# Kernel tuning notes

Measured on AMD Instinct MI355X. Metric: run time of the kernel, lower is better.

The kernel has to match this reference:

```python
import jax, jax.numpy as jnp
import numpy as np

LN_EPS = 1e-5
ALPHA_Q = 1.0

def _ln(t, g, b):
    mu = jnp.mean(t, -1, keepdims=True)
    var = jnp.var(t, -1, keepdims=True)
    return (t - mu) / jnp.sqrt(var + LN_EPS) * g + b

def _mlp(t, w1, b1, w2, b2):
    h = jax.nn.gelu(t @ w1.T + b1, approximate=False)
    return h @ w2.T + b2

def setup_inputs() -> dict:
    key = jax.random.key(0)
    B, N, L, E, H, D = 2, 2048, 2048, 1024, 16, 4
    ks = jax.random.split(key, 40)
    rn = lambda i, shape, sc: jax.random.normal(ks[i], shape, jnp.float32) * sc
    inp = {}
    inp['x'] = rn(0, (B, N, E), 1.0)
    inp['xp'] = jax.random.uniform(ks[1], (B, N, D), jnp.float32)
    inp['y'] = rn(2, (B, L, E), 1.0)
    inp['yp'] = jax.random.uniform(ks[3], (B, L, D), jnp.float32)
    inp['attn_mask'] = jax.random.uniform(ks[4], (1, 1, N, L), jnp.float32)
    # PositionEncoder params (torch Linear convention: weight [out,in])
    inp['p_w1'] = rn(5, (E, D), 1.0 / D)
    inp['p_b1'] = jax.random.uniform(ks[6], (E,), jnp.float32, 0.0, np.pi)
    inp['p_w2'] = rn(7, (E, D), 1.0 / D)
    inp['p_b2'] = jax.random.uniform(ks[8], (E,), jnp.float32, 0.0, np.pi)
    # QueryEncoder: LayerNorm + mlp1 + mlp2 (mlp0 is dead code in the source)
    inp['q_ln_g'] = jnp.ones((E,), jnp.float32); inp['q_ln_b'] = jnp.zeros((E,), jnp.float32)
    inp['q_m1_w1'] = rn(9, (2 * E, E), 0.02); inp['q_m1_b1'] = jnp.zeros((2 * E,), jnp.float32)
    inp['q_m1_w2'] = rn(10, (E, 2 * E), 0.02); inp['q_m1_b2'] = jnp.zeros((E,), jnp.float32)
    inp['q_m2_w1'] = rn(11, (2 * E, E), 0.02); inp['q_m2_b1'] = jnp.zeros((2 * E,), jnp.float32)
    inp['q_m2_w2'] = rn(12, (E, 2 * E), 0.02); inp['q_m2_b2'] = jnp.zeros((E,), jnp.float32)
    # KeyEncoder: LayerNorm + mlp1 (mlp0 dead code)
    inp['k_ln_g'] = jnp.ones((E,), jnp.float32); inp['k_ln_b'] = jnp.zeros((E,), jnp.float32)
    inp['k_m1_w1'] = rn(13, (2 * E, E), 0.02); inp['k_m1_b1'] = jnp.zeros((2 * E,), jnp.float32)
    inp['k_m1_w2'] = rn(14, (E, 2 * E), 0.02); inp['k_m1_b2'] = jnp.zeros((E,), jnp.float32)
    # V: LayerNorm + Linear
    inp['v_ln_g'] = jnp.ones((E,), jnp.float32); inp['v_ln_b'] = jnp.zeros((E,), jnp.float32)
    inp['v_w'] = rn(15, (E, E), 0.02); inp['v_b'] = jnp.zeros((E,), jnp.float32)
    # output projections
    inp['proj1_w'] = rn(16, (E, E), 0.02); inp['proj1_b'] = jnp.zeros((E,), jnp.float32)
    inp['proj2_w'] = rn(17, (E, D * H), 0.02); inp['proj2_b'] = jnp.zeros((E,), jnp.float32)
    return inp

def reference(x, xp, y, yp, attn_mask, p_w1, p_b1, p_w2, p_b2,
              q_ln_g, q_ln_b, q_m1_w1, q_m1_b1, q_m1_w2, q_m1_b2,
              q_m2_w1, q_m2_b1, q_m2_w2, q_m2_b2,
              k_ln_g, k_ln_b, k_m1_w1, k_m1_b1, k_m1_w2, k_m1_b2,
              v_ln_g, v_ln_b, v_w, v_b, proj1_w, proj1_b, proj2_w, proj2_b):
    B, N, E = x.shape
    L = y.shape[1]
    D = xp.shape[2]
    H = proj2_w.shape[1] // D
    C = E // H
    # PositionEncoder: query side with bias, key side without bias
    pxt = ALPHA_Q * xp
    xp1 = pxt @ p_w1.T + p_b1            # [B,N,E]
    xp2 = pxt @ p_w2.T + p_b2
    pyt = ALPHA_Q * yp
    yp1 = pyt @ p_w1.T                   # [B,L,E], no bias
    yp2 = pyt @ p_w2.T
    rh = lambda t: t.reshape(t.shape[0], -1, H, C)
    # QueryEncoder
    xn = _ln(x, q_ln_g, q_ln_b)
    x1 = _mlp(xn, q_m1_w1, q_m1_b1, q_m1_w2, q_m1_b2)
    x2 = _mlp(xn, q_m2_w1, q_m2_b1, q_m2_w2, q_m2_b2)
    q = jnp.concatenate([rh(x1 * jnp.cos(xp1)), rh(x1 * jnp.sin(xp1)),
                         rh(x2 * jnp.cos(xp2)), rh(x2 * jnp.sin(xp2))], axis=-1)  # [B,N,H,4C]
    # KeyEncoder (note: second cos/sin block is the raw position code)
    yn = _ln(y, k_ln_g, k_ln_b)
    y1 = _mlp(yn, k_m1_w1, k_m1_b1, k_m1_w2, k_m1_b2)
    k = jnp.concatenate([rh(y1 * jnp.cos(yp1)), rh(y1 * jnp.sin(yp1)),
                         rh(jnp.cos(yp2)), rh(jnp.sin(yp2))], axis=-1)            # [B,L,H,4C]
    scale = (4 * C) ** (-0.5)
    attn = jax.nn.softmax(jnp.einsum('bnhd,blhd->bhnl', q, k) * scale, axis=-1)
    # masked renormalization (mask applied AFTER softmax)
    eps = min(1e-8, 1.0 / L)
    attn = attn * attn_mask
    attn = attn / (jnp.sum(attn, axis=-1, keepdims=True) + eps)
    # values
    v = (_ln(y, v_ln_g, v_ln_b) @ v_w.T + v_b).reshape(B, L, H, C)
    out1 = jnp.einsum('bhnl,blhc->bnhc', attn, v).reshape(B, N, E) @ proj1_w.T + proj1_b
    out2 = jnp.einsum('bhnl,bld->bnhd', attn, yp) - xp[:, :, None, :]             # [B,N,H,D]
    out2 = out2.reshape(B, N, H * D) @ proj2_w.T + proj2_b
    return (out1 + out2, attn, xp)
```

## Files before the change

### kernel.cpp

```cpp
#include <hip/hip_runtime.h>
#include <math.h>
#include <stdint.h>

#define DEV static __device__ __forceinline__

typedef __bf16 bf16x8 __attribute__((ext_vector_type(8)));
typedef __bf16 bf16x4v __attribute__((ext_vector_type(4)));
typedef float f32x4 __attribute__((ext_vector_type(4)));

constexpr int Nn = 2048, Ll = 2048, Ee = 1024, Hh = 16;
constexpr float SCALE = 0.0625f;

constexpr size_t OFF_XN   = 0;
constexpr size_t OFF_YNK  = 8388608;
constexpr size_t OFF_YNV  = 16777216;
constexpr size_t OFF_H12  = 25165824;
constexpr size_t OFF_H3   = 58720256;
constexpr size_t OFF_X1   = 75497472;
constexpr size_t OFF_X2   = 83886080;
constexpr size_t OFF_Y1   = 92274688;
constexpr size_t OFF_QWS  = 100663296;
constexpr size_t OFF_KWS  = 134217728;
constexpr size_t OFF_VWS  = 167772160;
constexpr size_t OFF_DNV  = 176160768;
constexpr size_t OFF_YPT  = 176422912;
constexpr size_t OFF_MSK  = 176685056;
constexpr size_t OFF_AVZ  = 185073664;
constexpr size_t OFF_W1122= 193986560;
constexpr size_t OFF_W12  = 202375168;
constexpr size_t OFF_W22  = 206569472;
constexpr size_t OFF_WK1  = 210763776;
constexpr size_t OFF_WK2  = 214958080;
constexpr size_t OFF_WV   = 219152384;
constexpr size_t OFF_WP   = 221249536;
constexpr size_t OFF_EM   = 223477760;

DEV void gl2l(const void* g, void* l) {
  __builtin_amdgcn_global_load_lds((const __attribute__((address_space(1))) void*)g,
                                   (__attribute__((address_space(3))) void*)l, 16, 0, 0);
}

DEV float gelu_f(float v) {
  float x = v * 0.70710678118654752f;
  float ax = fabsf(x);
  float t = 1.f / fmaf(0.3275911f, ax, 1.f);
  float y = t * fmaf(t, fmaf(t, fmaf(t, fmaf(t, 1.061405429f, -1.453152027f),
                                     1.421413741f), -0.284496736f), 0.254829592f);
  float er = 1.f - y * __expf(-x * x);
  er = (x < 0.f) ? -er : er;
  return 0.5f * v * (1.f + er);
}

__launch_bounds__(256)
__global__ void prep_all(const float* __restrict__ s0, const float* __restrict__ s1,
                         const float* __restrict__ s2, const float* __restrict__ s3,
                         const float* __restrict__ s4, const float* __restrict__ s5,
                         const float* __restrict__ s6,
                         __bf16* __restrict__ d0, __bf16* __restrict__ d1,
                         __bf16* __restrict__ d2, __bf16* __restrict__ d3,
                         __bf16* __restrict__ d4, __bf16* __restrict__ d5,
                         __bf16* __restrict__ d6,
                         const float* __restrict__ pw1, const float* __restrict__ pw2,
                         __bf16* __restrict__ wp,
                         const float* __restrict__ mask, __bf16* __restrict__ mb,
                         const float* __restrict__ yp, __bf16* __restrict__ ypT) {
  int u = blockIdx.x * 256 + threadIdx.x;
  if (u < 3407872) {
    int seg = u >> 19, r = u & 524287;
    const float* s; __bf16* d;
    if      (seg == 0) { s = s0; d = d0; }
    else if (seg == 1) { s = s1; d = d1; }
    else if (seg == 2) { s = s2; d = d2; }
    else if (seg == 3) { s = s3; d = d3; }
    else if (seg == 4) { s = s4; d = d4; }
    else if (seg == 5) { s = s5; d = d5; }
    else               { s = s6; d = d6; }
    float4 v = ((const float4*)s)[r];
    bf16x4v o; o[0]=(__bf16)v.x; o[1]=(__bf16)v.y; o[2]=(__bf16)v.z; o[3]=(__bf16)v.w;
    ((bf16x4v*)d)[r] = o;
  } else if (u < 3686400) {
    int p = u - 3407872;
    int row = p / 272, c4 = p - row * 272;
    float4 v = (c4 < 256) ? ((const float4*)pw1)[row * 256 + c4]
                          : ((const float4*)pw2)[row * 16 + (c4 - 256)];
    bf16x4v o; o[0]=(__bf16)v.x; o[1]=(__bf16)v.y; o[2]=(__bf16)v.z; o[3]=(__bf16)v.w;
    *(bf16x4v*)(wp + (size_t)row * 1088 + (c4 << 2)) = o;
  } else if (u < 4734976) {
    int q = u - 3686400;
    float4 v = ((const float4*)mask)[q];
    bf16x4v o; o[0]=(__bf16)v.x; o[1]=(__bf16)v.y; o[2]=(__bf16)v.z; o[3]=(__bf16)v.w;
    ((bf16x4v*)mb)[q] = o;
  } else {
    int t0 = (u - 4734976) << 2;
    #pragma unroll
    for (int k = 0; k < 4; k++) {
      int i = t0 + k;
      int b = i >> 13, d = (i >> 11) & 3, l = i & 2047;
      ypT[i] = (__bf16)yp[(((size_t)b << 11) + l) * 4 + d];
    }
  }
}

__launch_bounds__(256)
__global__ void ln_all(const float* __restrict__ x, const float* __restrict__ y,
                       const float* __restrict__ qg, const float* __restrict__ qb,
                       const float* __restrict__ kg, const float* __restrict__ kb,
                       const float* __restrict__ vg, const float* __restrict__ vb,
                       __bf16* __restrict__ xn, __bf16* __restrict__ ynk,
                       __bf16* __restrict__ ynv) {
  const int t = blockIdx.x, tid = threadIdx.x;
  const bool isx = t < 4096;
  const int row = isx ? t : t - 4096;
  const float* src = (isx ? x : y) + (size_t)row * Ee;
  const float4 v = ((const float4*)src)[tid];
  float s = v.x + v.y + v.z + v.w;
  float q = v.x*v.x + v.y*v.y + v.z*v.z + v.w*v.w;
  #pragma unroll
  for (int o = 32; o > 0; o >>= 1) { s += __shfl_down(s, o); q += __shfl_down(q, o); }
  __shared__ float ls[4], lq[4];
  if ((tid & 63) == 0) { ls[tid >> 6] = s; lq[tid >> 6] = q; }
  __syncthreads();
  s = ls[0] + ls[1] + ls[2] + ls[3];
  q = lq[0] + lq[1] + lq[2] + lq[3];
  const float mu = s * (1.f / Ee);
  const float rstd = rsqrtf(q * (1.f / Ee) - mu * mu + 1e-5f);
  const int e0 = tid << 2;
  float h0 = (v.x - mu) * rstd, h1 = (v.y - mu) * rstd,
        h2 = (v.z - mu) * rstd, h3 = (v.w - mu) * rstd;
  if (isx) {
    bf16x4v o;
    o[0] = (__bf16)(h0 * qg[e0]   + qb[e0]);
    o[1] = (__bf16)(h1 * qg[e0+1] + qb[e0+1]);
    o[2] = (__bf16)(h2 * qg[e0+2] + qb[e0+2]);
    o[3] = (__bf16)(h3 * qg[e0+3] + qb[e0+3]);
    *(bf16x4v*)(xn + (size_t)row * Ee + e0) = o;
  } else {
    bf16x4v ok, ov;
    ok[0] = (__bf16)(h0 * kg[e0]   + kb[e0]);
    ok[1] = (__bf16)(h1 * kg[e0+1] + kb[e0+1]);
    ok[2] = (__bf16)(h2 * kg[e0+2] + kb[e0+2]);
    ok[3] = (__bf16)(h3 * kg[e0+3] + kb[e0+3]);
    ov[0] = (__bf16)(h0 * vg[e0]   + vb[e0]);
    ov[1] = (__bf16)(h1 * vg[e0+1] + vb[e0+1]);
    ov[2] = (__bf16)(h2 * vg[e0+2] + vb[e0+2]);
    ov[3] = (__bf16)(h3 * vg[e0+3] + vb[e0+3]);
    *(bf16x4v*)(ynk + (size_t)row * Ee + e0) = ok;
    *(bf16x4v*)(ynv + (size_t)row * Ee + e0) = ov;
  }
}


#define STAGE_A(BM_, A_, lda_, kt_, kh_, buf_)                                        \
  _Pragma("unroll")                                                                   \
  for (int jj = 0; jj < (BM_) / 128; jj++) {                                          \
    int c = (jj << 9) + tid;                                                          \
    int row_ = c >> 2, j_ = c & 3;                                                    \
    int col_ = ((kt_) << 6) + ((kh_) << 5) + ((j_ ^ (row_ & 3)) << 3);                \
    gl2l(A_ + (size_t)(m0 + row_) * (lda_) + col_,                                    \
         As + ((((buf_) << 1) + (kh_)) * ((BM_) * 32)) + (c << 3));                   \
  }

#define STAGE_B(W_, ldw_, kt_, kh_, buf_)                                             \
  _Pragma("unroll")                                                                   \
  for (int jj = 0; jj < 2; jj++) {                                                    \
    int c = (jj << 9) + tid;                                                          \
    int row_ = c >> 2, j_ = c & 3;                                                    \
    int col_ = ((kt_) << 6) + ((kh_) << 5) + ((j_ ^ (row_ & 3)) << 3);                \
    gl2l(W_ + (size_t)(n0 + row_) * (ldw_) + col_,                                    \
         Bs + ((((buf_) << 1) + (kh_)) * 8192) + (c << 3));                           \
  }

#define LOAD_A(BM_, buf_, ks_)                                                        \
  _Pragma("unroll")                                                                   \
  for (int i = 0; i < (BM_) / 32; i++) {                                              \
    int ra = wm + (i << 4) + li;                                                      \
    af[i] = *(const bf16x8*)(As + ((((buf_) << 1) + (ks_)) * ((BM_) * 32))            \
             + ra * 32 + ((g ^ (ra & 3)) << 3));                                      \
  }

#define LOAD_B(buf_, ks_, qn_)                                                        \
  _Pragma("unroll")                                                                   \
  for (int jj = 0; jj < 2; jj++) {                                                    \
    int rb = wn + ((qn_) << 5) + (jj << 4) + li;                                      \
    bw[jj] = *(const bf16x8*)(Bs + ((((buf_) << 1) + (ks_)) * 8192)                   \
             + rb * 32 + ((g ^ (rb & 3)) << 3));                                      \
  }

#define MFMA_Q(BM_, qn_)                                                              \
  __builtin_amdgcn_s_setprio(1);                                                      \
  _Pragma("unroll")                                                                   \
  for (int i = 0; i < (BM_) / 32; i++) {                                              \
    acc[i][((qn_) << 1)]     = __builtin_amdgcn_mfma_f32_16x16x32_bf16(af[i], bw[0], acc[i][((qn_) << 1)], 0, 0, 0);     \
    acc[i][((qn_) << 1) + 1] = __builtin_amdgcn_mfma_f32_16x16x32_bf16(af[i], bw[1], acc[i][((qn_) << 1) + 1], 0, 0, 0); \
  }                                                                                   \
  __builtin_amdgcn_s_setprio(0);

#define PH_SYNC                                                                       \
  __builtin_amdgcn_s_barrier();                                                       \
  asm volatile("s_waitcnt lgkmcnt(0)" ::: "memory");                                  \
  __builtin_amdgcn_sched_barrier(0);

#define PH_END __builtin_amdgcn_s_barrier();

#define GEMM_PIPE(BM_, A_, lda_, W_, ldw_, K_)                                        \
  const int w = tid >> 6, lane = tid & 63, g = lane >> 4, li = lane & 15;             \
  const int wm = (w >> 2) * ((BM_) / 2), wn = (w & 3) << 6;                           \
  constexpr int MI_ = (BM_) / 32;                                                     \
  constexpr int VMC = (BM_) / 128 + 2;                                                \
  f32x4 acc[MI_][4];                                                                  \
  _Pragma("unroll")                                                                   \
  for (int i = 0; i < MI_; i++)                                                       \
    _Pragma("unroll")                                                                 \
    for (int j = 0; j < 4; j++) acc[i][j] = (f32x4)0.f;                               \
                                    \
  STAGE_A(BM_, A_, lda_, 0, 0, 0) STAGE_B(W_, ldw_, 0, 0, 0)                          \
  STAGE_A(BM_, A_, lda_, 0, 1, 0) STAGE_B(W_, ldw_, 0, 1, 0)                          \
  STAGE_A(BM_, A_, lda_, 1, 0, 1) STAGE_B(W_, ldw_, 1, 0, 1)                          \
  asm volatile("s_waitcnt vmcnt(%0)" :: "i"(VMC) : "memory");                         \
  __builtin_amdgcn_s_barrier();                                                       \
  const int NT = (K_) >> 6;                                                           \
  bf16x8 af[MI_], bw[2];                                                              \
  for (int t = 0; t < NT; t++) {                                                      \
    const int buf = t & 1, nbuf = buf ^ 1;                                            \
    const bool sB = (t + 1 < NT);                     \
    const bool sA = (t + 2 < NT);                     \
                                                            \
    LOAD_A(BM_, buf, 0) LOAD_B(buf, 0, 0)                                             \
    if (sB) { STAGE_A(BM_, A_, lda_, t + 1, 1, nbuf) }                                \
    PH_SYNC MFMA_Q(BM_, 0) PH_END                                                     \
                                                 \
    LOAD_B(buf, 0, 1)                                                                 \
    if (sB) {                                                                         \
      STAGE_B(W_, ldw_, t + 1, 1, nbuf)                                               \
      asm volatile("s_waitcnt vmcnt(%0)" :: "i"(VMC) : "memory");                     \
    } else {                                                                          \
      asm volatile("s_waitcnt vmcnt(0)" ::: "memory");                                \
    }                                                                                 \
    PH_SYNC MFMA_Q(BM_, 1) PH_END                                                     \
                \
    LOAD_A(BM_, buf, 1) LOAD_B(buf, 1, 0)                                             \
    if (sA) { STAGE_A(BM_, A_, lda_, t + 2, 0, buf) }                                 \
    PH_SYNC MFMA_Q(BM_, 0) PH_END                                                     \
                                                            \
    LOAD_B(buf, 1, 1)                                                                 \
    if (sA) {                                                                         \
      STAGE_B(W_, ldw_, t + 2, 0, buf)                                                \
      asm volatile("s_waitcnt vmcnt(%0)" :: "i"(VMC) : "memory");                     \
    } else if (t + 1 < NT) {                                                          \
      asm volatile("s_waitcnt vmcnt(0)" ::: "memory");                                \
    }                                                                                 \
    PH_SYNC MFMA_Q(BM_, 1) PH_END                                                     \
  }

__launch_bounds__(512, 2)
__global__ void gemm_mlp1(const __bf16* __restrict__ xn, const __bf16* __restrict__ ynk,
                          const __bf16* __restrict__ w1122, const __bf16* __restrict__ wk1,
                          const float* __restrict__ qb1, const float* __restrict__ qb2,
                          const float* __restrict__ kb1,
                          __bf16* __restrict__ h12, __bf16* __restrict__ h3) {
  __shared__ __align__(16) __bf16 As[2 * 2 * 256 * 32];
  __shared__ __align__(16) __bf16 Bs[2 * 2 * 256 * 32];
  const int tid = threadIdx.x, bid = blockIdx.x;
  if (bid < 256) {
    const int m0 = (bid >> 4) << 8, n0 = (bid & 15) << 8;
    GEMM_PIPE(256, xn, 1024, w1122, 1024, 1024)
    #pragma unroll
    for (int j = 0; j < 4; j++) {
      int n = n0 + wn + (j << 4) + li;
      float bias = (n < 2048) ? qb1[n] : qb2[n - 2048];
      #pragma unroll
      for (int i = 0; i < MI_; i++) {
        #pragma unroll
        for (int r = 0; r < 4; r++) {
          int m = m0 + wm + (i << 4) + (g << 2) + r;
          h12[(size_t)m * 4096 + n] = (__bf16)gelu_f(acc[i][j][r] + bias);
        }
      }
    }
  } else {
    const int rr = bid - 256;
    const int m0 = (rr >> 3) << 7, n0 = (rr & 7) << 8;
    GEMM_PIPE(128, ynk, 1024, wk1, 1024, 1024)
    #pragma unroll
    for (int j = 0; j < 4; j++) {
      int n = n0 + wn + (j << 4) + li;
      float bias = kb1[n];
      #pragma unroll
      for (int i = 0; i < MI_; i++) {
        #pragma unroll
        for (int r = 0; r < 4; r++) {
          int m = m0 + wm + (i << 4) + (g << 2) + r;
          h3[(size_t)m * 2048 + n] = (__bf16)gelu_f(acc[i][j][r] + bias);
        }
      }
    }
  }
}

__launch_bounds__(512, 2)
__global__ void gemm_mlp2(const __bf16* __restrict__ h12, const __bf16* __restrict__ h3,
                          const __bf16* __restrict__ ynv,
                          const __bf16* __restrict__ w12, const __bf16* __restrict__ w22,
                          const __bf16* __restrict__ wk2, const __bf16* __restrict__ wv,
                          const float* __restrict__ bx1, const float* __restrict__ bx2,
                          const float* __restrict__ by1, const float* __restrict__ bv,
                          __bf16* __restrict__ x1, __bf16* __restrict__ x2,
                          __bf16* __restrict__ y1, __bf16* __restrict__ vT) {
  __shared__ __align__(16) __bf16 As[2 * 2 * 256 * 32];
  __shared__ __align__(16) __bf16 Bs[2 * 2 * 256 * 32];
  const int tid = threadIdx.x, bid = blockIdx.x;
  const int seg = bid >> 6, rr = bid & 63;
  const int m0 = (rr >> 2) << 8, n0 = (rr & 3) << 8;
  const __bf16* A; const __bf16* W; const float* bias; __bf16* out; int lda, K;
  if      (seg == 0) { A = h12;        lda = 4096; W = w12; bias = bx1; out = x1; K = 2048; }
  else if (seg == 1) { A = h12 + 2048; lda = 4096; W = w22; bias = bx2; out = x2; K = 2048; }
  else if (seg == 2) { A = h3;         lda = 2048; W = wk2; bias = by1; out = y1; K = 2048; }
  else               { A = ynv;        lda = 1024; W = wv;  bias = bv;  out = vT; K = 1024; }
  GEMM_PIPE(256, A, lda, W, K, K)
  #pragma unroll
  for (int j = 0; j < 4; j++) {
    int n = n0 + wn + (j << 4) + li;
    float bs = bias[n];
    #pragma unroll
    for (int i = 0; i < MI_; i++) {
      #pragma unroll
      for (int r = 0; r < 4; r++) {
        int m = m0 + wm + (i << 4) + (g << 2) + r;
        float v = acc[i][j][r] + bs;
        if (seg == 3) {
          int bb = m >> 11, l = m & 2047, hh = n >> 6, cc = n & 63;
          vT[(((size_t)(bb * Hh + hh) * 64 + cc) << 11) + l] = (__bf16)v;
        } else {
          out[(size_t)m * 1024 + n] = (__bf16)v;
        }
      }
    }
  }
}

__launch_bounds__(256)
__global__ void build_qk(const __bf16* __restrict__ x1, const __bf16* __restrict__ x2,
                         const float* __restrict__ xp,
                         const __bf16* __restrict__ y1, const float* __restrict__ yp,
                         const float* __restrict__ pw1, const float* __restrict__ pb1,
                         const float* __restrict__ pw2, const float* __restrict__ pb2,
                         __bf16* __restrict__ q_ws, __bf16* __restrict__ k_ws) {
  const bool isq = blockIdx.x < 2048;
  const int bid = isq ? blockIdx.x : blockIdx.x - 2048;
  const int t = (bid << 1) + (threadIdx.x >> 7);
  const int tl = threadIdx.x & 127;
  const int b = t >> 11, n = t & 2047;
  const int hh = tl >> 3, ch = tl & 7;
  const int e0 = (hh << 6) + (ch << 3);
  const float* pos = isq ? xp : yp;
  const float p0 = pos[(size_t)t*4], p1 = pos[(size_t)t*4+1],
              p2 = pos[(size_t)t*4+2], p3 = pos[(size_t)t*4+3];
  bf16x8 o0, o1, o2, o3;
  if (isq) {
    bf16x8 v1 = *(const bf16x8*)(x1 + (size_t)t * Ee + e0);
    bf16x8 v2 = *(const bf16x8*)(x2 + (size_t)t * Ee + e0);
    #pragma unroll
    for (int sub = 0; sub < 8; sub++) {
      int e = e0 + sub;
      float a1 = pw1[e*4]*p0 + pw1[e*4+1]*p1 + pw1[e*4+2]*p2 + pw1[e*4+3]*p3 + pb1[e];
      float a2 = pw2[e*4]*p0 + pw2[e*4+1]*p1 + pw2[e*4+2]*p2 + pw2[e*4+3]*p3 + pb2[e];
      float s1, c1, s2, c2;
      __sincosf(a1, &s1, &c1); __sincosf(a2, &s2, &c2);
      float xv1 = (float)v1[sub], xv2 = (float)v2[sub];
      o0[sub] = (__bf16)(xv1 * c1); o1[sub] = (__bf16)(xv1 * s1);
      o2[sub] = (__bf16)(xv2 * c2); o3[sub] = (__bf16)(xv2 * s2);
    }
  } else {
    bf16x8 v1 = *(const bf16x8*)(y1 + (size_t)t * Ee + e0);
    #pragma unroll
    for (int sub = 0; sub < 8; sub++) {
      int e = e0 + sub;
      float a1 = pw1[e*4]*p0 + pw1[e*4+1]*p1 + pw1[e*4+2]*p2 + pw1[e*4+3]*p3;
      float a2 = pw2[e*4]*p0 + pw2[e*4+1]*p1 + pw2[e*4+2]*p2 + pw2[e*4+3]*p3;
      float s1, c1, s2, c2;
      __sincosf(a1, &s1, &c1); __sincosf(a2, &s2, &c2);
      float yv = (float)v1[sub];
      o0[sub] = (__bf16)(yv * c1); o1[sub] = (__bf16)(yv * s1);
      o2[sub] = (__bf16)c2;        o3[sub] = (__bf16)s2;
    }
  }
  const int k = n & 7, bc = ch ^ k;
  __bf16* base = (isq ? q_ws : k_ws) + ((((size_t)b * Hh + hh) * Nn + n) << 8);
  *(bf16x8*)(base + ((bc          ) << 3)) = o0;
  *(bf16x8*)(base + (((8  ^ k) ^ ch) << 3)) = o1;
  *(bf16x8*)(base + (((16 ^ k) ^ ch) << 3)) = o2;
  *(bf16x8*)(base + (((24 ^ k) ^ ch) << 3)) = o3;
}

__launch_bounds__(512, 1)
__global__ void attn_fused(const __bf16* __restrict__ q_ws, const __bf16* __restrict__ k_ws,
                           const __bf16* __restrict__ vT_ws, const __bf16* __restrict__ ypT_g,
                           const __bf16* __restrict__ mask_bf, const float* __restrict__ xp,
                           __bf16* __restrict__ em_g, float* __restrict__ dinv_g,
                           __bf16* __restrict__ avz) {
  __shared__ __align__(16) __bf16 kq[2][32 * 256];
  __shared__ __align__(16) __bf16 ms[2][256 * 32];
  __shared__ __align__(16) __bf16 vt[2][64 * 40];
  __shared__ __align__(16) __bf16 pT[256 * 40];
  __shared__ __align__(16) __bf16 ypl[2][16 * 40];
  const int tid = threadIdx.x, w = tid >> 6, lane = tid & 63, g = lane >> 4, li = lane & 15;
  const int logical = ((blockIdx.x & 7) << 5) + (blockIdx.x >> 3);
  const int bh = logical >> 3, nt = logical & 7;
  const int b = bh >> 4, h = bh & 15;
  const int n0 = nt << 8;
  const __bf16* qb = q_ws + (((size_t)bh * Nn + n0) << 8);
  const __bf16* kb = k_ws + (((size_t)bh * Ll) << 8);
  const __bf16* vb = vT_ws + ((size_t)bh << 17);
  const __bf16* yb = ypT_g + ((size_t)b << 13);
  const __bf16* mb = mask_bf + ((size_t)n0 << 11);

  bf16x8 aq[2][8];
  #pragma unroll
  for (int rf = 0; rf < 2; rf++) {
    const int nloc = (w << 5) + (rf << 4) + li;
    #pragma unroll
    for (int s = 0; s < 8; s++)
      aq[rf][s] = *(const bf16x8*)(qb + ((size_t)nloc << 8) + ((((s << 2) + g) ^ (nloc & 7)) << 3));
  }
  for (int i = tid; i < 960; i += 512) {
    int buf = i / 480, idx = i - buf * 480;
    ypl[buf][160 + idx] = (__bf16)0.f;
  }
  {
    const int vc = tid >> 3, vl = (tid & 7) << 2;
    bf16x4v vreg = *(const bf16x4v*)(vb + ((size_t)vc << 11) + vl);
    bf16x4v ypreg;
    if (tid < 32) ypreg = *(const bf16x4v*)(yb + ((size_t)(tid >> 3) << 11) + ((tid & 7) << 2));
    #pragma unroll
    for (int j = 0; j < 2; j++) {
      int c = (j << 9) + tid;
      gl2l(kb + (size_t)(c >> 5) * 256 + ((c & 31) << 3), kq[0] + ((c - lane) << 3));
      gl2l(mb + (size_t)(c >> 2) * 2048 + ((c & 3) << 3), ms[0] + ((c - lane) << 3));
    }
    *(bf16x4v*)(vt[0] + vc * 40 + vl) = vreg;
    if (tid < 32) *(bf16x4v*)(ypl[0] + (tid >> 3) * 40 + ((tid & 7) << 2)) = ypreg;
  }
  __syncthreads();

  float se[2][4], te[2][4];
  f32x4 accv[2][4], accp[2];
  #pragma unroll
  for (int rf = 0; rf < 2; rf++) {
    #pragma unroll
    for (int r = 0; r < 4; r++) { se[rf][r] = 0.f; te[rf][r] = 0.f; }
    #pragma unroll
    for (int cb = 0; cb < 4; cb++) accv[rf][cb] = (f32x4)0.f;
    accp[rf] = (f32x4)0.f;
  }

  for (int t = 0; t < 64; ++t) {
    const int l0 = t << 5, cur = t & 1, nxt = cur ^ 1;
    const bool more = (t < 63);
    bf16x4v vreg, ypreg;
    if (more) {
      const int l1 = l0 + 32;
      vreg = *(const bf16x4v*)(vb + ((size_t)(tid >> 3) << 11) + l1 + ((tid & 7) << 2));
      if (tid < 32) ypreg = *(const bf16x4v*)(yb + ((size_t)(tid >> 3) << 11) + l1 + ((tid & 7) << 2));
      #pragma unroll
      for (int j = 0; j < 2; j++) {
        int c = (j << 9) + tid;
        gl2l(kb + (size_t)(l1 + (c >> 5)) * 256 + ((c & 31) << 3), kq[nxt] + ((c - lane) << 3));
        gl2l(mb + (size_t)(c >> 2) * 2048 + l1 + ((c & 3) << 3), ms[nxt] + ((c - lane) << 3));
      }
    }
    f32x4 Cs[2][2];
    Cs[0][0] = (f32x4)0.f; Cs[0][1] = (f32x4)0.f; Cs[1][0] = (f32x4)0.f; Cs[1][1] = (f32x4)0.f;
    #pragma unroll
    for (int lb = 0; lb < 2; lb++) {
      const int kr = (lb << 4) + li;
      #pragma unroll
      for (int s = 0; s < 8; s++) {
        bf16x8 bk = *(const bf16x8*)(kq[cur] + kr * 256 + ((((s << 2) + g) ^ (kr & 7)) << 3));
        Cs[0][lb] = __builtin_amdgcn_mfma_f32_16x16x32_bf16(aq[0][s], bk, Cs[0][lb], 0, 0, 0);
        Cs[1][lb] = __builtin_amdgcn_mfma_f32_16x16x32_bf16(aq[1][s], bk, Cs[1][lb], 0, 0, 0);
      }
    }
    #pragma unroll
    for (int rf = 0; rf < 2; rf++) {
      #pragma unroll
      for (int lb = 0; lb < 2; lb++) {
        #pragma unroll
        for (int r = 0; r < 4; r++) {
          const int row = (w << 5) + (rf << 4) + (g << 2) + r;
          float e = __expf(Cs[rf][lb][r] * SCALE);
          float mkv = (float)ms[cur][row * 32 + (lb << 4) + li];
          float em = e * mkv;
          se[rf][r] += e; te[rf][r] += em;
          pT[row * 40 + (lb << 4) + li] = (__bf16)em;
        }
      }
    }
    asm volatile("s_waitcnt lgkmcnt(0)" ::: "memory");
    __builtin_amdgcn_sched_barrier(0);
    #pragma unroll
    for (int j = 0; j < 2; j++) {
      int q = (j << 6) + lane;
      int row = q >> 2, ch = q & 3;
      bf16x8 pv = *(const bf16x8*)(pT + ((w << 5) + row) * 40 + (ch << 3));
      *(bf16x8*)(em_g + ((size_t)bh << 22) + ((size_t)(n0 + (w << 5) + row) << 11) + l0 + (ch << 3)) = pv;
    }
    bf16x8 vv[4];
    #pragma unroll
    for (int cb = 0; cb < 4; cb++)
      vv[cb] = *(const bf16x8*)(vt[cur] + ((cb << 4) + li) * 40 + (g << 3));
    bf16x8 yy = *(const bf16x8*)(ypl[cur] + li * 40 + (g << 3));
    #pragma unroll
    for (int rf = 0; rf < 2; rf++) {
      bf16x8 pa = *(const bf16x8*)(pT + ((w << 5) + (rf << 4) + li) * 40 + (g << 3));
      #pragma unroll
      for (int cb = 0; cb < 4; cb++)
        accv[rf][cb] = __builtin_amdgcn_mfma_f32_16x16x32_bf16(pa, vv[cb], accv[rf][cb], 0, 0, 0);
      accp[rf] = __builtin_amdgcn_mfma_f32_16x16x32_bf16(pa, yy, accp[rf], 0, 0, 0);
    }
    if (more) {
      *(bf16x4v*)(vt[nxt] + (tid >> 3) * 40 + ((tid & 7) << 2)) = vreg;
      if (tid < 32) *(bf16x4v*)(ypl[nxt] + (tid >> 3) * 40 + ((tid & 7) << 2)) = ypreg;
    }
    __syncthreads();
  }

  #pragma unroll
  for (int rf = 0; rf < 2; rf++) {
    #pragma unroll
    for (int r = 0; r < 4; r++) {
      float s = se[rf][r], tt = te[rf][r];
      #pragma unroll
      for (int o = 1; o < 16; o <<= 1) { s += __shfl_xor(s, o); tt += __shfl_xor(tt, o); }
      float dinv = 1.f / (tt + 1e-8f * s);
      const int n = n0 + (w << 5) + (rf << 4) + (g << 2) + r;
      if (li == 0) dinv_g[((size_t)bh << 11) + n] = dinv;
      #pragma unroll
      for (int cb = 0; cb < 4; cb++)
        avz[((size_t)b * Nn + n) * 1088 + (h << 6) + (cb << 4) + li] = (__bf16)(accv[rf][cb][r] * dinv);
      if (li < 4) {
        float z = accp[rf][r] * dinv - xp[(((size_t)b * Nn + n) << 2) + li];
        avz[((size_t)b * Nn + n) * 1088 + 1024 + (h << 2) + li] = (__bf16)z;
      }
    }
  }
}

__launch_bounds__(256)
__global__ void fin_proj(const __bf16* __restrict__ A, const __bf16* __restrict__ W,
                         const float* __restrict__ bias1, const float* __restrict__ bias2,
                         float* __restrict__ out,
                         const __bf16* __restrict__ em_g, const float* __restrict__ dinv_g,
                         float* __restrict__ attn_out,
                         const float* __restrict__ xp, float* __restrict__ xp_out) {
  constexpr int N = 1024, K = 1088;
  __shared__ __align__(16) __bf16 As[2][128 * 32];
  __shared__ __align__(16) __bf16 Bs[2][64 * 32];
  const int tid = threadIdx.x;
  if (blockIdx.x >= 512) {
    const int sbid = blockIdx.x - 512;
    if (sbid < 64) {
      int idx = sbid * 256 + tid;
      ((float4*)xp_out)[idx] = ((const float4*)xp)[idx];
    }
    for (size_t i8 = sbid * 256ul + tid; i8 < 16777216ul; i8 += 524288ul) {
      bf16x8 v = ((const bf16x8*)em_g)[i8];
      float dv = dinv_g[i8 >> 8];
      float4 o0, o1;
      o0.x = (float)v[0] * dv; o0.y = (float)v[1] * dv; o0.z = (float)v[2] * dv; o0.w = (float)v[3] * dv;
      o1.x = (float)v[4] * dv; o1.y = (float)v[5] * dv; o1.z = (float)v[6] * dv; o1.w = (float)v[7] * dv;
      ((float4*)attn_out)[i8 * 2]     = o0;
      ((float4*)attn_out)[i8 * 2 + 1] = o1;
    }
    return;
  }
  const int w = tid >> 6, lane = tid & 63, g = lane >> 4, li = lane & 15;
  const int bt = blockIdx.x >> 4;
  const int m0 = bt << 7, n0 = (blockIdx.x & 15) << 6;
  const int wm = (w >> 1) << 6, wn = (w & 1) << 5;
  f32x4 acc[4][2];
  #pragma unroll
  for (int i = 0; i < 4; i++) { acc[i][0] = (f32x4)0.f; acc[i][1] = (f32x4)0.f; }
  auto stage = [&](int buf, int kt) {
    const int col0 = kt << 5;
    #pragma unroll
    for (int j = 0; j < 2; j++) {
      int c = (j << 8) + tid;
      int row = c >> 2, sl = c & 3;
      int col = col0 + ((sl ^ (row & 3)) << 3);
      gl2l(A + (size_t)(m0 + row) * K + col, As[buf] + ((c - lane) << 3));
    }
    {
      int c = tid;
      int row = c >> 2, sl = c & 3;
      int col = col0 + ((sl ^ (row & 3)) << 3);
      gl2l(W + (size_t)(n0 + row) * K + col, Bs[buf] + ((c - lane) << 3));
    }
  };
  const int NT = K >> 5;
  stage(0, 0);
  for (int kt = 0; kt < NT; kt++) {
    const int cur = kt & 1;
    if (kt + 1 < NT) {
      stage(cur ^ 1, kt + 1);
      asm volatile("s_waitcnt vmcnt(3)" ::: "memory");
    } else {
      asm volatile("s_waitcnt vmcnt(0)" ::: "memory");
    }
    __builtin_amdgcn_s_barrier();
    __builtin_amdgcn_sched_barrier(0);
    bf16x8 af[4], bw[2];
    #pragma unroll
    for (int i = 0; i < 4; i++) {
      int ra = wm + (i << 4) + li;
      af[i] = *(const bf16x8*)(As[cur] + ra * 32 + ((g ^ (ra & 3)) << 3));
    }
    #pragma unroll
    for (int j = 0; j < 2; j++) {
      int rb = wn + (j << 4) + li;
      bw[j] = *(const bf16x8*)(Bs[cur] + rb * 32 + ((g ^ (rb & 3)) << 3));
    }
    #pragma unroll
    for (int i = 0; i < 4; i++)
      #pragma unroll
      for (int j = 0; j < 2; j++)
        acc[i][j] = __builtin_amdgcn_mfma_f32_16x16x32_bf16(af[i], bw[j], acc[i][j], 0, 0, 0);
    asm volatile("s_waitcnt lgkmcnt(0)" ::: "memory");
    __builtin_amdgcn_sched_barrier(0);
    __builtin_amdgcn_s_barrier();
  }
  #pragma unroll
  for (int j = 0; j < 2; j++) {
    int n = n0 + wn + (j << 4) + li;
    float bias = bias1[n] + bias2[n];
    #pragma unroll
    for (int i = 0; i < 4; i++) {
      #pragma unroll
      for (int r = 0; r < 4; r++) {
        int m = m0 + wm + (i << 4) + (g << 2) + r;
        out[(size_t)m * N + n] = acc[i][j][r] + bias;
      }
    }
  }
}

extern "C" void kernel_launch(void* const* d_in, const int* in_sizes, int n_in,
                              void* d_out, int out_size, void* d_ws, size_t ws_size,
                              hipStream_t stream) {
  (void)in_sizes; (void)n_in; (void)out_size; (void)ws_size;
  const float* x       = (const float*)d_in[0];
  const float* xp      = (const float*)d_in[1];
  const float* y       = (const float*)d_in[2];
  const float* yp      = (const float*)d_in[3];
  const float* mask    = (const float*)d_in[4];
  const float* p_w1    = (const float*)d_in[5];
  const float* p_b1    = (const float*)d_in[6];
  const float* p_w2    = (const float*)d_in[7];
  const float* p_b2    = (const float*)d_in[8];
  const float* q_ln_g  = (const float*)d_in[9];
  const float* q_ln_b  = (const float*)d_in[10];
  const float* q_m1_w1 = (const float*)d_in[11];
  const float* q_m1_b1 = (const float*)d_in[12];
  const float* q_m1_w2 = (const float*)d_in[13];
  const float* q_m1_b2 = (const float*)d_in[14];
  const float* q_m2_w1 = (const float*)d_in[15];
  const float* q_m2_b1 = (const float*)d_in[16];
  const float* q_m2_w2 = (const float*)d_in[17];
  const float* q_m2_b2 = (const float*)d_in[18];
  const float* k_ln_g  = (const float*)d_in[19];
  const float* k_ln_b  = (const float*)d_in[20];
  const float* k_m1_w1 = (const float*)d_in[21];
  const float* k_m1_b1 = (const float*)d_in[22];
  const float* k_m1_w2 = (const float*)d_in[23];
  const float* k_m1_b2 = (const float*)d_in[24];
  const float* v_ln_g  = (const float*)d_in[25];
  const float* v_ln_b  = (const float*)d_in[26];
  const float* v_w     = (const float*)d_in[27];
  const float* v_b     = (const float*)d_in[28];
  const float* proj1_w = (const float*)d_in[29];
  const float* proj1_b = (const float*)d_in[30];
  const float* proj2_w = (const float*)d_in[31];
  const float* proj2_b = (const float*)d_in[32];

  char* ws = (char*)d_ws;
  __bf16* xn    = (__bf16*)(ws + OFF_XN);
  __bf16* ynk   = (__bf16*)(ws + OFF_YNK);
  __bf16* ynv   = (__bf16*)(ws + OFF_YNV);
  __bf16* h12   = (__bf16*)(ws + OFF_H12);
  __bf16* h3    = (__bf16*)(ws + OFF_H3);
  __bf16* x1    = (__bf16*)(ws + OFF_X1);
  __bf16* x2    = (__bf16*)(ws + OFF_X2);
  __bf16* y1    = (__bf16*)(ws + OFF_Y1);
  __bf16* q_ws  = (__bf16*)(ws + OFF_QWS);
  __bf16* k_ws  = (__bf16*)(ws + OFF_KWS);
  __bf16* vT_ws = (__bf16*)(ws + OFF_VWS);
  float*  dinv  = (float*)(ws + OFF_DNV);
  __bf16* ypT   = (__bf16*)(ws + OFF_YPT);
  __bf16* mskb  = (__bf16*)(ws + OFF_MSK);
  __bf16* avz   = (__bf16*)(ws + OFF_AVZ);
  __bf16* w1122 = (__bf16*)(ws + OFF_W1122);
  __bf16* w12   = (__bf16*)(ws + OFF_W12);
  __bf16* w22   = (__bf16*)(ws + OFF_W22);
  __bf16* wk1   = (__bf16*)(ws + OFF_WK1);
  __bf16* wk2   = (__bf16*)(ws + OFF_WK2);
  __bf16* wv    = (__bf16*)(ws + OFF_WV);
  __bf16* wp    = (__bf16*)(ws + OFF_WP);
  __bf16* em    = (__bf16*)(ws + OFF_EM);

  float* out0     = (float*)d_out;
  float* attn_out = out0 + (size_t)4194304;
  float* xp_out   = out0 + (size_t)138412032;

  prep_all<<<18512, 256, 0, stream>>>(q_m1_w1, q_m2_w1, q_m1_w2, q_m2_w2, k_m1_w1, k_m1_w2, v_w,
                                      w1122, w1122 + 2097152, w12, w22, wk1, wk2, wv,
                                      proj1_w, proj2_w, wp, mask, mskb, yp, ypT);
  ln_all<<<8192, 256, 0, stream>>>(x, y, q_ln_g, q_ln_b, k_ln_g, k_ln_b, v_ln_g, v_ln_b,
                                   xn, ynk, ynv);
  gemm_mlp1<<<512, 512, 0, stream>>>(xn, ynk, w1122, wk1, q_m1_b1, q_m2_b1, k_m1_b1, h12, h3);
  gemm_mlp2<<<256, 512, 0, stream>>>(h12, h3, ynv, w12, w22, wk2, wv,
                                     q_m1_b2, q_m2_b2, k_m1_b2, v_b, x1, x2, y1, vT_ws);
  build_qk<<<4096, 256, 0, stream>>>(x1, x2, xp, y1, yp, p_w1, p_b1, p_w2, p_b2, q_ws, k_ws);
  attn_fused<<<256, 512, 0, stream>>>(q_ws, k_ws, vT_ws, ypT, mskb, xp, em, dinv, avz);
  fin_proj<<<2560, 256, 0, stream>>>(avz, wp, proj1_b, proj2_b, out0,
                                     em, dinv, attn_out, xp, xp_out);
}
```

Measured before the change: 694.5 us.

## Merge prep and layernorm launches; load mask into registers in attention

The weight/mask conversion kernel and the layernorm kernel become one launch, with extra blocks doing the layernorm work, which removes a launch boundary. In the fused attention kernel the mask tile is no longer staged through LDS with async global-to-LDS copies. Each thread now loads its mask values directly into registers and applies the mask during the vectorized write-out of probabilities. The masked row sums are reduced through shuffles and a small shared array. This frees LDS and cuts LDS traffic, at the cost of extra register pressure, an added lgkmcnt wait, and synchronous global mask loads on the critical path.

```diff
diff --git a/kernel.cpp b/kernel.cpp
--- a/kernel.cpp
+++ b/kernel.cpp
@@ -52,19 +52,68 @@
 }
 
 __launch_bounds__(256)
-__global__ void prep_all(const float* __restrict__ s0, const float* __restrict__ s1,
-                         const float* __restrict__ s2, const float* __restrict__ s3,
-                         const float* __restrict__ s4, const float* __restrict__ s5,
-                         const float* __restrict__ s6,
-                         __bf16* __restrict__ d0, __bf16* __restrict__ d1,
-                         __bf16* __restrict__ d2, __bf16* __restrict__ d3,
-                         __bf16* __restrict__ d4, __bf16* __restrict__ d5,
-                         __bf16* __restrict__ d6,
-                         const float* __restrict__ pw1, const float* __restrict__ pw2,
-                         __bf16* __restrict__ wp,
-                         const float* __restrict__ mask, __bf16* __restrict__ mb,
-                         const float* __restrict__ yp, __bf16* __restrict__ ypT) {
-  int u = blockIdx.x * 256 + threadIdx.x;
+__global__ void prep_ln(const float* __restrict__ s0, const float* __restrict__ s1,
+                        const float* __restrict__ s2, const float* __restrict__ s3,
+                        const float* __restrict__ s4, const float* __restrict__ s5,
+                        const float* __restrict__ s6,
+                        __bf16* __restrict__ d0, __bf16* __restrict__ d1,
+                        __bf16* __restrict__ d2, __bf16* __restrict__ d3,
+                        __bf16* __restrict__ d4, __bf16* __restrict__ d5,
+                        __bf16* __restrict__ d6,
+                        const float* __restrict__ pw1, const float* __restrict__ pw2,
+                        __bf16* __restrict__ wp,
+                        const float* __restrict__ mask, __bf16* __restrict__ mb,
+                        const float* __restrict__ yp, __bf16* __restrict__ ypT,
+                        const float* __restrict__ x, const float* __restrict__ y,
+                        const float* __restrict__ qg, const float* __restrict__ qb,
+                        const float* __restrict__ kg, const float* __restrict__ kb,
+                        const float* __restrict__ vg, const float* __restrict__ vb,
+                        __bf16* __restrict__ xn, __bf16* __restrict__ ynk,
+                        __bf16* __restrict__ ynv) {
+  const int tid = threadIdx.x;
+  if (blockIdx.x >= 18512) {
+    const int t = blockIdx.x - 18512;
+    const bool isx = t < 4096;
+    const int row = isx ? t : t - 4096;
+    const float* src = (isx ? x : y) + (size_t)row * Ee;
+    const float4 v = ((const float4*)src)[tid];
+    float s = v.x + v.y + v.z + v.w;
+    float q = v.x*v.x + v.y*v.y + v.z*v.z + v.w*v.w;
+    #pragma unroll
+    for (int o = 32; o > 0; o >>= 1) { s += __shfl_down(s, o); q += __shfl_down(q, o); }
+    __shared__ float ls[4], lq[4];
+    if ((tid & 63) == 0) { ls[tid >> 6] = s; lq[tid >> 6] = q; }
+    __syncthreads();
+    s = ls[0] + ls[1] + ls[2] + ls[3];
+    q = lq[0] + lq[1] + lq[2] + lq[3];
+    const float mu = s * (1.f / Ee);
+    const float rstd = rsqrtf(q * (1.f / Ee) - mu * mu + 1e-5f);
+    const int e0 = tid << 2;
+    float h0 = (v.x - mu) * rstd, h1 = (v.y - mu) * rstd,
+          h2 = (v.z - mu) * rstd, h3 = (v.w - mu) * rstd;
+    if (isx) {
+      bf16x4v o;
+      o[0] = (__bf16)(h0 * qg[e0]   + qb[e0]);
+      o[1] = (__bf16)(h1 * qg[e0+1] + qb[e0+1]);
+      o[2] = (__bf16)(h2 * qg[e0+2] + qb[e0+2]);
+      o[3] = (__bf16)(h3 * qg[e0+3] + qb[e0+3]);
+      *(bf16x4v*)(xn + (size_t)row * Ee + e0) = o;
+    } else {
+      bf16x4v ok, ov;
+      ok[0] = (__bf16)(h0 * kg[e0]   + kb[e0]);
+      ok[1] = (__bf16)(h1 * kg[e0+1] + kb[e0+1]);
+      ok[2] = (__bf16)(h2 * kg[e0+2] + kb[e0+2]);
+      ok[3] = (__bf16)(h3 * kg[e0+3] + kb[e0+3]);
+      ov[0] = (__bf16)(h0 * vg[e0]   + vb[e0]);
+      ov[1] = (__bf16)(h1 * vg[e0+1] + vb[e0+1]);
+      ov[2] = (__bf16)(h2 * vg[e0+2] + vb[e0+2]);
+      ov[3] = (__bf16)(h3 * vg[e0+3] + vb[e0+3]);
+      *(bf16x4v*)(ynk + (size_t)row * Ee + e0) = ok;
+      *(bf16x4v*)(ynv + (size_t)row * Ee + e0) = ov;
+    }
+    return;
+  }
+  int u = blockIdx.x * 256 + tid;
   if (u < 3407872) {
     int seg = u >> 19, r = u & 524287;
     const float* s; __bf16* d;
@@ -101,55 +150,6 @@
   }
 }
 
-__launch_bounds__(256)
-__global__ void ln_all(const float* __restrict__ x, const float* __restrict__ y,
-                       const float* __restrict__ qg, const float* __restrict__ qb,
-                       const float* __restrict__ kg, const float* __restrict__ kb,
-                       const float* __restrict__ vg, const float* __restrict__ vb,
-                       __bf16* __restrict__ xn, __bf16* __restrict__ ynk,
-                       __bf16* __restrict__ ynv) {
-  const int t = blockIdx.x, tid = threadIdx.x;
-  const bool isx = t < 4096;
-  const int row = isx ? t : t - 4096;
-  const float* src = (isx ? x : y) + (size_t)row * Ee;
-  const float4 v = ((const float4*)src)[tid];
-  float s = v.x + v.y + v.z + v.w;
-  float q = v.x*v.x + v.y*v.y + v.z*v.z + v.w*v.w;
-  #pragma unroll
-  for (int o = 32; o > 0; o >>= 1) { s += __shfl_down(s, o); q += __shfl_down(q, o); }
-  __shared__ float ls[4], lq[4];
-  if ((tid & 63) == 0) { ls[tid >> 6] = s; lq[tid >> 6] = q; }
-  __syncthreads();
-  s = ls[0] + ls[1] + ls[2] + ls[3];
-  q = lq[0] + lq[1] + lq[2] + lq[3];
-  const float mu = s * (1.f / Ee);
-  const float rstd = rsqrtf(q * (1.f / Ee) - mu * mu + 1e-5f);
-  const int e0 = tid << 2;
-  float h0 = (v.x - mu) * rstd, h1 = (v.y - mu) * rstd,
-        h2 = (v.z - mu) * rstd, h3 = (v.w - mu) * rstd;
-  if (isx) {
-    bf16x4v o;
-    o[0] = (__bf16)(h0 * qg[e0]   + qb[e0]);
-    o[1] = (__bf16)(h1 * qg[e0+1] + qb[e0+1]);
-    o[2] = (__bf16)(h2 * qg[e0+2] + qb[e0+2]);
-    o[3] = (__bf16)(h3 * qg[e0+3] + qb[e0+3]);
-    *(bf16x4v*)(xn + (size_t)row * Ee + e0) = o;
-  } else {
-    bf16x4v ok, ov;
-    ok[0] = (__bf16)(h0 * kg[e0]   + kb[e0]);
-    ok[1] = (__bf16)(h1 * kg[e0+1] + kb[e0+1]);
-    ok[2] = (__bf16)(h2 * kg[e0+2] + kb[e0+2]);
-    ok[3] = (__bf16)(h3 * kg[e0+3] + kb[e0+3]);
-    ov[0] = (__bf16)(h0 * vg[e0]   + vb[e0]);
-    ov[1] = (__bf16)(h1 * vg[e0+1] + vb[e0+1]);
-    ov[2] = (__bf16)(h2 * vg[e0+2] + vb[e0+2]);
-    ov[3] = (__bf16)(h3 * vg[e0+3] + vb[e0+3]);
-    *(bf16x4v*)(ynk + (size_t)row * Ee + e0) = ok;
-    *(bf16x4v*)(ynv + (size_t)row * Ee + e0) = ov;
-  }
-}
-
-
 #define STAGE_A(BM_, A_, lda_, kt_, kh_, buf_)                                        \
   _Pragma("unroll")                                                                   \
   for (int jj = 0; jj < (BM_) / 128; jj++) {                                          \
@@ -212,7 +212,6 @@
   for (int i = 0; i < MI_; i++)                                                       \
     _Pragma("unroll")                                                                 \
     for (int j = 0; j < 4; j++) acc[i][j] = (f32x4)0.f;                               \
-                                    \
   STAGE_A(BM_, A_, lda_, 0, 0, 0) STAGE_B(W_, ldw_, 0, 0, 0)                          \
   STAGE_A(BM_, A_, lda_, 0, 1, 0) STAGE_B(W_, ldw_, 0, 1, 0)                          \
   STAGE_A(BM_, A_, lda_, 1, 0, 1) STAGE_B(W_, ldw_, 1, 0, 1)                          \
@@ -222,13 +221,11 @@
   bf16x8 af[MI_], bw[2];                                                              \
   for (int t = 0; t < NT; t++) {                                                      \
     const int buf = t & 1, nbuf = buf ^ 1;                                            \
-    const bool sB = (t + 1 < NT);                     \
-    const bool sA = (t + 2 < NT);                     \
-                                                            \
+    const bool sB = (t + 1 < NT);                                                     \
+    const bool sA = (t + 2 < NT);                                                     \
     LOAD_A(BM_, buf, 0) LOAD_B(buf, 0, 0)                                             \
     if (sB) { STAGE_A(BM_, A_, lda_, t + 1, 1, nbuf) }                                \
     PH_SYNC MFMA_Q(BM_, 0) PH_END                                                     \
-                                                 \
     LOAD_B(buf, 0, 1)                                                                 \
     if (sB) {                                                                         \
       STAGE_B(W_, ldw_, t + 1, 1, nbuf)                                               \
@@ -237,11 +234,9 @@
       asm volatile("s_waitcnt vmcnt(0)" ::: "memory");                                \
     }                                                                                 \
     PH_SYNC MFMA_Q(BM_, 1) PH_END                                                     \
-                \
     LOAD_A(BM_, buf, 1) LOAD_B(buf, 1, 0)                                             \
     if (sA) { STAGE_A(BM_, A_, lda_, t + 2, 0, buf) }                                 \
     PH_SYNC MFMA_Q(BM_, 0) PH_END                                                     \
-                                                            \
     LOAD_B(buf, 1, 1)                                                                 \
     if (sA) {                                                                         \
       STAGE_B(W_, ldw_, t + 2, 0, buf)                                                \
@@ -399,10 +394,10 @@
                            __bf16* __restrict__ em_g, float* __restrict__ dinv_g,
                            __bf16* __restrict__ avz) {
   __shared__ __align__(16) __bf16 kq[2][32 * 256];
-  __shared__ __align__(16) __bf16 ms[2][256 * 32];
   __shared__ __align__(16) __bf16 vt[2][64 * 40];
   __shared__ __align__(16) __bf16 pT[256 * 40];
   __shared__ __align__(16) __bf16 ypl[2][16 * 40];
+  __shared__ float te_s[256];
   const int tid = threadIdx.x, w = tid >> 6, lane = tid & 63, g = lane >> 4, li = lane & 15;
   const int logical = ((blockIdx.x & 7) << 5) + (blockIdx.x >> 3);
   const int bh = logical >> 3, nt = logical & 7;
@@ -414,6 +409,8 @@
   const __bf16* yb = ypT_g + ((size_t)b << 13);
   const __bf16* mb = mask_bf + ((size_t)n0 << 11);
 
+  const int srow = lane >> 2, sch = lane & 3;
+
   bf16x8 aq[2][8];
   #pragma unroll
   for (int rf = 0; rf < 2; rf++) {
@@ -435,19 +432,19 @@
     for (int j = 0; j < 2; j++) {
       int c = (j << 9) + tid;
       gl2l(kb + (size_t)(c >> 5) * 256 + ((c & 31) << 3), kq[0] + ((c - lane) << 3));
-      gl2l(mb + (size_t)(c >> 2) * 2048 + ((c & 3) << 3), ms[0] + ((c - lane) << 3));
     }
     *(bf16x4v*)(vt[0] + vc * 40 + vl) = vreg;
     if (tid < 32) *(bf16x4v*)(ypl[0] + (tid >> 3) * 40 + ((tid & 7) << 2)) = ypreg;
   }
   __syncthreads();
 
-  float se[2][4], te[2][4];
+  float se[2][4];
+  float teq0 = 0.f, teq1 = 0.f;
   f32x4 accv[2][4], accp[2];
   #pragma unroll
   for (int rf = 0; rf < 2; rf++) {
     #pragma unroll
-    for (int r = 0; r < 4; r++) { se[rf][r] = 0.f; te[rf][r] = 0.f; }
+    for (int r = 0; r < 4; r++) se[rf][r] = 0.f;
     #pragma unroll
     for (int cb = 0; cb < 4; cb++) accv[rf][cb] = (f32x4)0.f;
     accp[rf] = (f32x4)0.f;
@@ -456,6 +453,8 @@
   for (int t = 0; t < 64; ++t) {
     const int l0 = t << 5, cur = t & 1, nxt = cur ^ 1;
     const bool more = (t < 63);
+    bf16x8 mk0 = *(const bf16x8*)(mb + (size_t)((w << 5) + srow) * 2048 + l0 + (sch << 3));
+    bf16x8 mk1 = *(const bf16x8*)(mb + (size_t)((w << 5) + 16 + srow) * 2048 + l0 + (sch << 3));
     bf16x4v vreg, ypreg;
     if (more) {
       const int l1 = l0 + 32;
@@ -465,7 +464,6 @@
       for (int j = 0; j < 2; j++) {
         int c = (j << 9) + tid;
         gl2l(kb + (size_t)(l1 + (c >> 5)) * 256 + ((c & 31) << 3), kq[nxt] + ((c - lane) << 3));
-        gl2l(mb + (size_t)(c >> 2) * 2048 + l1 + ((c & 3) << 3), ms[nxt] + ((c - lane) << 3));
       }
     }
     f32x4 Cs[2][2];
@@ -488,10 +486,8 @@
         for (int r = 0; r < 4; r++) {
           const int row = (w << 5) + (rf << 4) + (g << 2) + r;
           float e = __expf(Cs[rf][lb][r] * SCALE);
-          float mkv = (float)ms[cur][row * 32 + (lb << 4) + li];
-          float em = e * mkv;
-          se[rf][r] += e; te[rf][r] += em;
-          pT[row * 40 + (lb << 4) + li] = (__bf16)em;
+          se[rf][r] += e;
+          pT[row * 40 + (lb << 4) + li] = (__bf16)e;
         }
       }
     }
@@ -499,11 +495,25 @@
     __builtin_amdgcn_sched_barrier(0);
     #pragma unroll
     for (int j = 0; j < 2; j++) {
-      int q = (j << 6) + lane;
-      int row = q >> 2, ch = q & 3;
-      bf16x8 pv = *(const bf16x8*)(pT + ((w << 5) + row) * 40 + (ch << 3));
-      *(bf16x8*)(em_g + ((size_t)bh << 22) + ((size_t)(n0 + (w << 5) + row) << 11) + l0 + (ch << 3)) = pv;
-    }
+      const int row = (j << 4) + srow;
+      bf16x8 pv = *(const bf16x8*)(pT + ((w << 5) + row) * 40 + (sch << 3));
+      bf16x8 mk = j ? mk1 : mk0;
+      bf16x8 emv;
+      float tp = 0.f;
+      #pragma unroll
+      for (int i = 0; i < 8; i++) {
+        float p = (float)pv[i] * (float)mk[i];
+        emv[i] = (__bf16)p;
+        tp += p;
+      }
+      tp += __shfl_xor(tp, 1);
+      tp += __shfl_xor(tp, 2);
+      if (j) teq1 += tp; else teq0 += tp;
+      *(bf16x8*)(em_g + ((size_t)bh << 22) + ((size_t)(n0 + (w << 5) + row) << 11) + l0 + (sch << 3)) = emv;
+      *(bf16x8*)(pT + ((w << 5) + row) * 40 + (sch << 3)) = emv;
+    }
+    asm volatile("s_waitcnt lgkmcnt(0)" ::: "memory");
+    __builtin_amdgcn_sched_barrier(0);
     bf16x8 vv[4];
     #pragma unroll
     for (int cb = 0; cb < 4; cb++)
@@ -524,13 +534,22 @@
     __syncthreads();
   }
 
+  if ((lane & 3) == 0) {
+    te_s[(w << 5) + srow]      = teq0;
+    te_s[(w << 5) + 16 + srow] = teq1;
+  }
+  asm volatile("s_waitcnt lgkmcnt(0)" ::: "memory");
+  __builtin_amdgcn_sched_barrier(0);
+  __syncthreads();
+
   #pragma unroll
   for (int rf = 0; rf < 2; rf++) {
     #pragma unroll
     for (int r = 0; r < 4; r++) {
-      float s = se[rf][r], tt = te[rf][r];
-      #pragma unroll
-      for (int o = 1; o < 16; o <<= 1) { s += __shfl_xor(s, o); tt += __shfl_xor(tt, o); }
+      float s = se[rf][r];
+      #pragma unroll
+      for (int o = 1; o < 16; o <<= 1) s += __shfl_xor(s, o);
+      float tt = te_s[(w << 5) + (rf << 4) + (g << 2) + r];
       float dinv = 1.f / (tt + 1e-8f * s);
       const int n = n0 + (w << 5) + (rf << 4) + (g << 2) + r;
       if (li == 0) dinv_g[((size_t)bh << 11) + n] = dinv;
@@ -710,11 +729,11 @@
   float* attn_out = out0 + (size_t)4194304;
   float* xp_out   = out0 + (size_t)138412032;
 
-  prep_all<<<18512, 256, 0, stream>>>(q_m1_w1, q_m2_w1, q_m1_w2, q_m2_w2, k_m1_w1, k_m1_w2, v_w,
-                                      w1122, w1122 + 2097152, w12, w22, wk1, wk2, wv,
-                                      proj1_w, proj2_w, wp, mask, mskb, yp, ypT);
-  ln_all<<<8192, 256, 0, stream>>>(x, y, q_ln_g, q_ln_b, k_ln_g, k_ln_b, v_ln_g, v_ln_b,
-                                   xn, ynk, ynv);
+  prep_ln<<<26704, 256, 0, stream>>>(q_m1_w1, q_m2_w1, q_m1_w2, q_m2_w2, k_m1_w1, k_m1_w2, v_w,
+                                     w1122, w1122 + 2097152, w12, w22, wk1, wk2, wv,
+                                     proj1_w, proj2_w, wp, mask, mskb, yp, ypT,
+                                     x, y, q_ln_g, q_ln_b, k_ln_g, k_ln_b, v_ln_g, v_ln_b,
+                                     xn, ynk, ynv);
   gemm_mlp1<<<512, 512, 0, stream>>>(xn, ynk, w1122, wk1, q_m1_b1, q_m2_b1, k_m1_b1, h12, h3);
   gemm_mlp2<<<256, 512, 0, stream>>>(h12, h3, ynv, w12, w22, wk2, wv,
                                      q_m1_b2, q_m2_b2, k_m1_b2, v_b, x1, x2, y1, vT_ws);
```

Result: no change. 689.1 us (-0.8%).
